# Kernel tuning notes

Measured on AMD Instinct MI355X. Metric: run time of the kernel, lower is better.

## Reference

```python
import jax, jax.numpy as jnp
import numpy as np

M, N, D = 8192, 8192, 64

def setup_inputs() -> dict:
    key = jax.random.key(0)
    k1, k2 = jax.random.split(key)
    X = jax.random.normal(k1, (M, D), dtype=jnp.float32)
    Y = jax.random.normal(k2, (N, D), dtype=jnp.float32)
    gamma_param = jnp.asarray(1.0, dtype=jnp.float32)  # learnable scalar (rbf branch)
    return {"X": X, "Y": Y, "gamma_param": gamma_param}

def reference(X, Y, gamma_param):
    # RBF kernel: exp(-gamma * ||x_i - y_j||^2), (m, n)
    x_sq = jnp.sum(X * X, axis=-1)          # (m,)
    y_sq = jnp.sum(Y * Y, axis=-1)          # (n,)
    xy = jnp.einsum("md,nd->mn", X, Y)      # (m, n)
    sq_norm = x_sq[:, None] + y_sq[None, :] - 2.0 * xy
    sq_norm = jnp.maximum(sq_norm, 0.0)     # numerical clamp
    return jnp.exp(-gamma_param * sq_norm)
```

## Files before the change

### kernel.cpp

```cpp
#include <hip/hip_runtime.h>

#define MTOT 8192
#define NTOT 8192
#define DD   64
#define SPLIT (MTOT * DD)

typedef __bf16 bf16x8 __attribute__((ext_vector_type(8)));
typedef float  f32x16 __attribute__((ext_vector_type(16)));
typedef unsigned short u16;
typedef unsigned short u16x4 __attribute__((ext_vector_type(4)));
typedef unsigned short u16x8 __attribute__((ext_vector_type(8)));

__device__ __forceinline__ u16 bf16_rne(float v) {
    unsigned int u = __float_as_uint(v);
    u = u + 0x7FFFu + ((u >> 16) & 1u);
    return (u16)(u >> 16);
}
__device__ __forceinline__ float bf16_to_f32(u16 h) {
    return __uint_as_float(((unsigned int)h) << 16);
}

#define MFMA(a, b, c) __builtin_amdgcn_mfma_f32_32x32x16_bf16((a), (b), (c), 0, 0, 0)

__global__ __launch_bounds__(256)
void rbf_pre_kernel(const float* __restrict__ X, const float* __restrict__ Y,
                    u16* __restrict__ XhiF, u16* __restrict__ XloF,
                    u16* __restrict__ YhiF, u16* __restrict__ YloF,
                    float* __restrict__ xqs, float* __restrict__ yqs)
{
    const int gid = blockIdx.x * 256 + threadIdx.x;
    const int mat = gid >> 15;
    const int r4  = gid & 32767;
    const int row = r4 >> 2;
    const int q   = r4 & 3;
    const float* src = mat ? Y : X;
    u16* hi  = mat ? YhiF : XhiF;
    u16* lo  = mat ? YloF : XloF;
    float* nrm = mat ? yqs : xqs;

    const long rbase = (long)row * DD + q * 16;
    float s = 0.f;
    u16x8 h0, h1, l0, l1;
    #pragma unroll
    for (int c = 0; c < 4; ++c) {
        const float4 v = *reinterpret_cast<const float4*>(src + rbase + c * 4);
        const float vv[4] = {v.x, v.y, v.z, v.w};
        #pragma unroll
        for (int e = 0; e < 4; ++e) {
            const int idx = c * 4 + e;
            const float x = vv[e];
            s = fmaf(x, x, s);
            const u16 hh = bf16_rne(x);
            const u16 ll = bf16_rne(x - bf16_to_f32(hh));
            if (idx < 8) { h0[idx] = hh; l0[idx] = ll; }
            else         { h1[idx - 8] = hh; l1[idx - 8] = ll; }
        }
    }
    s += __shfl_xor(s, 1);
    s += __shfl_xor(s, 2);
    if (q == 0) nrm[row] = s;

    const int tt = row >> 5, lr = row & 31;
    const long fbase = (long)(tt * 4 + q) * 512;
    *reinterpret_cast<u16x8*>(hi + fbase + lr * 8)        = h0;
    *reinterpret_cast<u16x8*>(hi + fbase + (32 + lr) * 8) = h1;
    *reinterpret_cast<u16x8*>(lo + fbase + lr * 8)        = l0;
    *reinterpret_cast<u16x8*>(lo + fbase + (32 + lr) * 8) = l1;
}

__global__ __launch_bounds__(256, 4)
void rbf_hiocc_kernel(const u16* __restrict__ XhiF, const u16* __restrict__ XloF,
                      const u16* __restrict__ YhiF, const u16* __restrict__ YloF,
                      const float* __restrict__ xqs, const float* __restrict__ yqs,
                      const float* __restrict__ gamma_p,
                      float* __restrict__ out)
{
    __shared__ __align__(16) u16 S[2][8192];

    const int t = threadIdx.x;
    const int w = t >> 6;
    const int l = t & 63;
    const int loff = l * 8;

    const int bid = blockIdx.x;
    const int swz = ((bid & 7) << 10) | (bid >> 3);
    const int bm = swz >> 6;
    const int bn = swz & 63;
    const long row0 = (long)bm * 64;
    const long col0 = (long)bn * 128;

    {
        const u16* const yh = YhiF + (long)bn * 8192;
        const u16* const yl = YloF + (long)bn * 8192;
        #pragma unroll
        for (int cc = 0; cc < 8; ++cc) {
            const int c = w * 8 + cc;
            const u16* gsrc = (c < 16) ? (yh + c * 512) : (yl + (c - 16) * 512);
            u16* ldst = (c < 16) ? &S[0][c * 512] : &S[1][(c - 16) * 512];
            *reinterpret_cast<int4*>(ldst + loff) = *reinterpret_cast<const int4*>(gsrc + loff);
        }
    }

    const int mt  = w & 1;
    const int nt0 = (w >> 1) * 2;

    const long att = (long)(bm * 2 + mt);
    bf16x8 aH[4], aL[4];
    #pragma unroll
    for (int ks = 0; ks < 4; ++ks) {
        aH[ks] = *reinterpret_cast<const bf16x8*>(XhiF + (att * 4 + ks) * 512 + loff);
        aL[ks] = *reinterpret_cast<const bf16x8*>(XloF + (att * 4 + ks) * 512 + loff);
    }

    const float g  = gamma_p[0];
    const float g2 = 2.0f * g;
    const int l5x4 = (l >> 5) * 4;
    const int  ln  = l & 31;

    float xv[16];
    #pragma unroll
    for (int q4 = 0; q4 < 4; ++q4) {
        const float4 x4 = *reinterpret_cast<const float4*>(
            xqs + row0 + mt * 32 + 8 * q4 + l5x4);
        xv[q4 * 4 + 0] = x4.x; xv[q4 * 4 + 1] = x4.y;
        xv[q4 * 4 + 2] = x4.z; xv[q4 * 4 + 3] = x4.w;
    }
    const float cy0 = -g * yqs[col0 + (nt0 + 0) * 32 + ln];
    const float cy1 = -g * yqs[col0 + (nt0 + 1) * 32 + ln];

    __syncthreads();

    f32x16 acc0, acc1;
    #pragma unroll
    for (int r = 0; r < 16; ++r) { acc0[r] = 0.f; acc1[r] = 0.f; }

    #pragma unroll
    for (int ks = 0; ks < 4; ++ks) {
        const bf16x8 b0h = *reinterpret_cast<const bf16x8*>(&S[0][((nt0 + 0) * 4 + ks) * 512 + loff]);
        const bf16x8 b1h = *reinterpret_cast<const bf16x8*>(&S[0][((nt0 + 1) * 4 + ks) * 512 + loff]);
        const bf16x8 b0l = *reinterpret_cast<const bf16x8*>(&S[1][((nt0 + 0) * 4 + ks) * 512 + loff]);
        const bf16x8 b1l = *reinterpret_cast<const bf16x8*>(&S[1][((nt0 + 1) * 4 + ks) * 512 + loff]);
        acc0 = MFMA(aH[ks], b0h, acc0);
        acc1 = MFMA(aH[ks], b1h, acc1);
        acc0 = MFMA(aH[ks], b0l, acc0);
        acc1 = MFMA(aH[ks], b1l, acc1);
        acc0 = MFMA(aL[ks], b0h, acc0);
        acc1 = MFMA(aL[ks], b1h, acc1);
    }

    float* const obase = out + (row0 + mt * 32) * (long)NTOT + col0 + nt0 * 32 + ln;
    #pragma unroll
    for (int r = 0; r < 16; ++r) {
        const int rr = (r & 3) + 8 * (r >> 2) + l5x4;
        float* const orow = obase + rr * (long)NTOT;
        const float a0 = fminf(fmaf(g2, acc0[r], fmaf(-g, xv[r], cy0)), 0.f);
        const float a1 = fminf(fmaf(g2, acc1[r], fmaf(-g, xv[r], cy1)), 0.f);
        orow[0]  = __expf(a0);
        orow[32] = __expf(a1);
    }
}

__global__ __launch_bounds__(256, 2)
void rbf_fallback_kernel(const float* __restrict__ X,
                         const float* __restrict__ Y,
                         const float* __restrict__ gamma_p,
                         float* __restrict__ out)
{
    __shared__ unsigned short XfH[4][4][64][8];
    __shared__ unsigned short XfL[4][4][64][8];
    __shared__ unsigned short YfH[4][4][64][8];
    __shared__ unsigned short YfL[4][4][64][8];
    __shared__ float xq[128];
    __shared__ float yq[128];

    const int t = threadIdx.x;
    const long row0 = (long)blockIdx.y * 128;
    const long col0 = (long)blockIdx.x * 128;

    {
        const int k0   = (t & 15) * 4;
        const int ks   = k0 >> 4;
        const int l32  = ((k0 >> 3) & 1) << 5;
        const int slot = k0 & 4;
        #pragma unroll
        for (int i = 0; i < 8; ++i) {
            const int row  = (t >> 4) + i * 16;
            const int mt   = row >> 5;
            const int lane = (row & 31) | l32;
            const float4 vx = *reinterpret_cast<const float4*>(X + (row0 + row) * DD + k0);
            const float4 vy = *reinterpret_cast<const float4*>(Y + (col0 + row) * DD + k0);
            float xv[4] = {vx.x, vx.y, vx.z, vx.w};
            float yv[4] = {vy.x, vy.y, vy.z, vy.w};
            u16x4 xh, xl, yh, yl;
            #pragma unroll
            for (int e = 0; e < 4; ++e) {
                const u16 hx = bf16_rne(xv[e]);
                xh[e] = hx; xl[e] = bf16_rne(xv[e] - bf16_to_f32(hx));
                const u16 hy = bf16_rne(yv[e]);
                yh[e] = hy; yl[e] = bf16_rne(yv[e] - bf16_to_f32(hy));
            }
            *reinterpret_cast<u16x4*>(&XfH[mt][ks][lane][slot]) = xh;
            *reinterpret_cast<u16x4*>(&XfL[mt][ks][lane][slot]) = xl;
            *reinterpret_cast<u16x4*>(&YfH[mt][ks][lane][slot]) = yh;
            *reinterpret_cast<u16x4*>(&YfL[mt][ks][lane][slot]) = yl;
        }
    }
    {
        const int r = t & 127;
        const float* p2 = (t < 128) ? (X + (row0 + r) * DD) : (Y + (col0 + r) * DD);
        float s0 = 0.f, s1 = 0.f, s2 = 0.f, s3 = 0.f;
        #pragma unroll
        for (int c = 0; c < 16; ++c) {
            const float4 v = reinterpret_cast<const float4*>(p2)[c];
            s0 = fmaf(v.x, v.x, s0); s1 = fmaf(v.y, v.y, s1);
            s2 = fmaf(v.z, v.z, s2); s3 = fmaf(v.w, v.w, s3);
        }
        const float s = (s0 + s1) + (s2 + s3);
        if (t < 128) xq[r] = s; else yq[r] = s;
    }
    __syncthreads();

    const int w = t >> 6;
    const int l = t & 63;
    const int mt0 = (w >> 1) * 2;
    const int nt0 = (w & 1) * 2;

    bf16x8 aH[2][4], aL[2][4];
    #pragma unroll
    for (int i = 0; i < 2; ++i)
        #pragma unroll
        for (int ks = 0; ks < 4; ++ks) {
            aH[i][ks] = *reinterpret_cast<const bf16x8*>(&XfH[mt0 + i][ks][l][0]);
            aL[i][ks] = *reinterpret_cast<const bf16x8*>(&XfL[mt0 + i][ks][l][0]);
        }

    f32x16 acc[2][2];
    #pragma unroll
    for (int i = 0; i < 2; ++i)
        #pragma unroll
        for (int j = 0; j < 2; ++j)
            #pragma unroll
            for (int r = 0; r < 16; ++r) acc[i][j][r] = 0.f;

    #pragma unroll
    for (int ks = 0; ks < 4; ++ks) {
        const bf16x8 b0h = *reinterpret_cast<const bf16x8*>(&YfH[nt0 + 0][ks][l][0]);
        const bf16x8 b1h = *reinterpret_cast<const bf16x8*>(&YfH[nt0 + 1][ks][l][0]);
        const bf16x8 b0l = *reinterpret_cast<const bf16x8*>(&YfL[nt0 + 0][ks][l][0]);
        const bf16x8 b1l = *reinterpret_cast<const bf16x8*>(&YfL[nt0 + 1][ks][l][0]);
        acc[0][0] = MFMA(aH[0][ks], b0h, acc[0][0]);
        acc[0][1] = MFMA(aH[0][ks], b1h, acc[0][1]);
        acc[1][0] = MFMA(aH[1][ks], b0h, acc[1][0]);
        acc[1][1] = MFMA(aH[1][ks], b1h, acc[1][1]);
        acc[0][0] = MFMA(aH[0][ks], b0l, acc[0][0]);
        acc[0][1] = MFMA(aH[0][ks], b1l, acc[0][1]);
        acc[1][0] = MFMA(aH[1][ks], b0l, acc[1][0]);
        acc[1][1] = MFMA(aH[1][ks], b1l, acc[1][1]);
        acc[0][0] = MFMA(aL[0][ks], b0h, acc[0][0]);
        acc[0][1] = MFMA(aL[0][ks], b1h, acc[0][1]);
        acc[1][0] = MFMA(aL[1][ks], b0h, acc[1][0]);
        acc[1][1] = MFMA(aL[1][ks], b1h, acc[1][1]);
    }

    const float g = gamma_p[0];
    const int l5x4 = (l >> 5) * 4;
    const int ln = l & 31;
    #pragma unroll
    for (int i = 0; i < 2; ++i) {
        const int mt = mt0 + i;
        float xv[16];
        #pragma unroll
        for (int r = 0; r < 16; ++r)
            xv[r] = xq[mt * 32 + (r & 3) + 8 * (r >> 2) + l5x4];
        #pragma unroll
        for (int j = 0; j < 2; ++j) {
            const int nt = nt0 + j;
            const float yv = yq[nt * 32 + ln];
            const long gr = row0 + mt * 32;
            const long gc = col0 + nt * 32 + ln;
            #pragma unroll
            for (int r = 0; r < 16; ++r) {
                float s = fmaf(-2.f, acc[i][j][r], xv[r] + yv);
                s = fmaxf(s, 0.f);
                const long rr = gr + (r & 3) + 8 * (r >> 2) + l5x4;
                out[rr * NTOT + gc] = __expf(-g * s);
            }
        }
    }
}

extern "C" void kernel_launch(void* const* d_in, const int* in_sizes, int n_in,
                              void* d_out, int out_size, void* d_ws, size_t ws_size,
                              hipStream_t stream) {
    (void)in_sizes; (void)n_in; (void)out_size;
    const float* X = (const float*)d_in[0];
    const float* Y = (const float*)d_in[1];
    const float* gamma_p = (const float*)d_in[2];
    float* out = (float*)d_out;

    const size_t need = 4 * (size_t)SPLIT * sizeof(u16) + (MTOT + NTOT) * sizeof(float);

    if (ws_size >= need) {
        u16* XhiF = (u16*)d_ws;
        u16* XloF = XhiF + SPLIT;
        u16* YhiF = XloF + SPLIT;
        u16* YloF = YhiF + SPLIT;
        float* xqs = (float*)(YloF + SPLIT);
        float* yqs = xqs + MTOT;
        rbf_pre_kernel<<<256, 256, 0, stream>>>(X, Y, XhiF, XloF, YhiF, YloF, xqs, yqs);
        rbf_hiocc_kernel<<<8192, 256, 0, stream>>>(XhiF, XloF, YhiF, YloF, xqs, yqs, gamma_p, out);
    } else {
        dim3 grid(NTOT / 128, MTOT / 128);
        rbf_fallback_kernel<<<grid, 256, 0, stream>>>(X, Y, gamma_p, out);
    }
}
```

Before: 60.41 us.

## Use 128x128 tiles with LDS-staged vectorized nontemporal output stores

Doubles the block tile to 128 rows so each wave computes a full 32x128 strip and the shared Y tile is reused across four waves. The exp results are staged through a per-wave LDS buffer and written back as row-contiguous 16-byte nontemporal stores, replacing the earlier strided 4-byte stores. This targets the cost of the 256 MB output write. In exchange it uses 32 KB more LDS, lowers occupancy to 2 blocks per CU, and adds LDS round trips.

```diff
diff --git a/kernel.cpp b/kernel.cpp
--- a/kernel.cpp
+++ b/kernel.cpp
@@ -7,6 +7,7 @@
 
 typedef __bf16 bf16x8 __attribute__((ext_vector_type(8)));
 typedef float  f32x16 __attribute__((ext_vector_type(16)));
+typedef float  f32x4  __attribute__((ext_vector_type(4)));
 typedef unsigned short u16;
 typedef unsigned short u16x4 __attribute__((ext_vector_type(4)));
 typedef unsigned short u16x8 __attribute__((ext_vector_type(8)));
@@ -68,14 +69,15 @@
     *reinterpret_cast<u16x8*>(lo + fbase + (32 + lr) * 8) = l1;
 }
 
-__global__ __launch_bounds__(256, 4)
-void rbf_hiocc_kernel(const u16* __restrict__ XhiF, const u16* __restrict__ XloF,
-                      const u16* __restrict__ YhiF, const u16* __restrict__ YloF,
-                      const float* __restrict__ xqs, const float* __restrict__ yqs,
-                      const float* __restrict__ gamma_p,
-                      float* __restrict__ out)
+__global__ __launch_bounds__(256, 2)
+void rbf_t4_kernel(const u16* __restrict__ XhiF, const u16* __restrict__ XloF,
+                   const u16* __restrict__ YhiF, const u16* __restrict__ YloF,
+                   const float* __restrict__ xqs, const float* __restrict__ yqs,
+                   const float* __restrict__ gamma_p,
+                   float* __restrict__ out)
 {
     __shared__ __align__(16) u16 S[2][8192];
+    __shared__ __align__(16) float T[8192];
 
     const int t = threadIdx.x;
     const int w = t >> 6;
@@ -83,10 +85,10 @@
     const int loff = l * 8;
 
     const int bid = blockIdx.x;
-    const int swz = ((bid & 7) << 10) | (bid >> 3);
+    const int swz = ((bid & 7) << 9) | (bid >> 3);
     const int bm = swz >> 6;
     const int bn = swz & 63;
-    const long row0 = (long)bm * 64;
+    const long row0 = (long)bm * 128;
     const long col0 = (long)bn * 128;
 
     {
@@ -101,10 +103,7 @@
         }
     }
 
-    const int mt  = w & 1;
-    const int nt0 = (w >> 1) * 2;
-
-    const long att = (long)(bm * 2 + mt);
+    const long att = (long)(bm * 4 + w);
     bf16x8 aH[4], aL[4];
     #pragma unroll
     for (int ks = 0; ks < 4; ++ks) {
@@ -121,42 +120,66 @@
     #pragma unroll
     for (int q4 = 0; q4 < 4; ++q4) {
         const float4 x4 = *reinterpret_cast<const float4*>(
-            xqs + row0 + mt * 32 + 8 * q4 + l5x4);
+            xqs + row0 + w * 32 + 8 * q4 + l5x4);
         xv[q4 * 4 + 0] = x4.x; xv[q4 * 4 + 1] = x4.y;
         xv[q4 * 4 + 2] = x4.z; xv[q4 * 4 + 3] = x4.w;
     }
-    const float cy0 = -g * yqs[col0 + (nt0 + 0) * 32 + ln];
-    const float cy1 = -g * yqs[col0 + (nt0 + 1) * 32 + ln];
+    const float cy0 = -g * yqs[col0 +  0 + ln];
+    const float cy1 = -g * yqs[col0 + 32 + ln];
+    const float cy2 = -g * yqs[col0 + 64 + ln];
+    const float cy3 = -g * yqs[col0 + 96 + ln];
 
     __syncthreads();
 
-    f32x16 acc0, acc1;
-    #pragma unroll
-    for (int r = 0; r < 16; ++r) { acc0[r] = 0.f; acc1[r] = 0.f; }
-
-    #pragma unroll
-    for (int ks = 0; ks < 4; ++ks) {
-        const bf16x8 b0h = *reinterpret_cast<const bf16x8*>(&S[0][((nt0 + 0) * 4 + ks) * 512 + loff]);
-        const bf16x8 b1h = *reinterpret_cast<const bf16x8*>(&S[0][((nt0 + 1) * 4 + ks) * 512 + loff]);
-        const bf16x8 b0l = *reinterpret_cast<const bf16x8*>(&S[1][((nt0 + 0) * 4 + ks) * 512 + loff]);
-        const bf16x8 b1l = *reinterpret_cast<const bf16x8*>(&S[1][((nt0 + 1) * 4 + ks) * 512 + loff]);
-        acc0 = MFMA(aH[ks], b0h, acc0);
-        acc1 = MFMA(aH[ks], b1h, acc1);
-        acc0 = MFMA(aH[ks], b0l, acc0);
-        acc1 = MFMA(aH[ks], b1l, acc1);
-        acc0 = MFMA(aL[ks], b0h, acc0);
-        acc1 = MFMA(aL[ks], b1h, acc1);
-    }
-
-    float* const obase = out + (row0 + mt * 32) * (long)NTOT + col0 + nt0 * 32 + ln;
-    #pragma unroll
-    for (int r = 0; r < 16; ++r) {
-        const int rr = (r & 3) + 8 * (r >> 2) + l5x4;
-        float* const orow = obase + rr * (long)NTOT;
-        const float a0 = fminf(fmaf(g2, acc0[r], fmaf(-g, xv[r], cy0)), 0.f);
-        const float a1 = fminf(fmaf(g2, acc1[r], fmaf(-g, xv[r], cy1)), 0.f);
-        orow[0]  = __expf(a0);
-        orow[32] = __expf(a1);
+    f32x16 q0, q1, q2, q3;
+    #pragma unroll
+    for (int r = 0; r < 16; ++r) { q0[r] = 0.f; q1[r] = 0.f; q2[r] = 0.f; q3[r] = 0.f; }
+
+#define QUAD(ACC, JJ)                                                                       \
+    {                                                                                       \
+        _Pragma("unroll")                                                                   \
+        for (int ks = 0; ks < 4; ++ks) {                                                    \
+            const bf16x8 bh = *reinterpret_cast<const bf16x8*>(&S[0][((JJ) * 4 + ks) * 512 + loff]); \
+            const bf16x8 bl = *reinterpret_cast<const bf16x8*>(&S[1][((JJ) * 4 + ks) * 512 + loff]); \
+            ACC = MFMA(aH[ks], bh, ACC);                                                    \
+            ACC = MFMA(aH[ks], bl, ACC);                                                    \
+            ACC = MFMA(aL[ks], bh, ACC);                                                    \
+        }                                                                                   \
+    }
+    QUAD(q0, 0)
+    QUAD(q1, 1)
+    QUAD(q2, 2)
+    QUAD(q3, 3)
+#undef QUAD
+
+    float* const Tw = &T[w * 2048];
+    const int rofs = l >> 5;
+    const int c4   = ln * 4;
+
+    #pragma unroll
+    for (int p = 0; p < 2; ++p) {
+        #pragma unroll
+        for (int r8 = 0; r8 < 8; ++r8) {
+            const int r    = 8 * p + r8;
+            const int rloc = (r8 & 3) + 8 * (r8 >> 2) + l5x4;
+            const float nx = fmaf(-g, xv[r], 0.f);
+            float* const trow = Tw + rloc * 128 + ln;
+            trow[ 0] = __expf(fminf(fmaf(g2, q0[r], nx + cy0), 0.f));
+            trow[32] = __expf(fminf(fmaf(g2, q1[r], nx + cy1), 0.f));
+            trow[64] = __expf(fminf(fmaf(g2, q2[r], nx + cy2), 0.f));
+            trow[96] = __expf(fminf(fmaf(g2, q3[r], nx + cy3), 0.f));
+        }
+        __builtin_amdgcn_wave_barrier();
+
+        #pragma unroll
+        for (int k = 0; k < 8; ++k) {
+            const int rloc = 2 * k + rofs;
+            const f32x4 v = *reinterpret_cast<const f32x4*>(Tw + rloc * 128 + c4);
+            const long grow = row0 + w * 32 + p * 16 + rloc;
+            __builtin_nontemporal_store(v,
+                reinterpret_cast<f32x4*>(out + grow * (long)NTOT + col0 + c4));
+        }
+        __builtin_amdgcn_wave_barrier();
     }
 }
 
@@ -308,7 +331,7 @@
         float* xqs = (float*)(YloF + SPLIT);
         float* yqs = xqs + MTOT;
         rbf_pre_kernel<<<256, 256, 0, stream>>>(X, Y, XhiF, XloF, YhiF, YloF, xqs, yqs);
-        rbf_hiocc_kernel<<<8192, 256, 0, stream>>>(XhiF, XloF, YhiF, YloF, xqs, yqs, gamma_p, out);
+        rbf_t4_kernel<<<4096, 256, 0, stream>>>(XhiF, XloF, YhiF, YloF, xqs, yqs, gamma_p, out);
     } else {
         dim3 grid(NTOT / 128, MTOT / 128);
         rbf_fallback_kernel<<<grid, 256, 0, stream>>>(X, Y, gamma_p, out);
```

New measurement: 60.59 us. About the same (+0.3%).
